# Kernel tuning notes

Measured on AMD Instinct MI355X. Metric: run time of the kernel, lower is better.

Reference implementation:

```python
import jax, jax.numpy as jnp
import numpy as np

N = 500000
E = 3000000
F = 128


def _lin_params(key, fan_in, fan_out):
    kw, kb = jax.random.split(key)
    s = 1.0 / np.sqrt(fan_in)
    w = jax.random.uniform(kw, (fan_in, fan_out), jnp.float32, -s, s)
    b = jax.random.uniform(kb, (fan_out,), jnp.float32, -s, s)
    return w, b


def setup_inputs() -> dict:
    key = jax.random.key(0)
    ks = jax.random.split(key, 16)
    hv = jax.random.normal(ks[0], (N, 7), jnp.float32)
    edge_index = jax.random.randint(ks[1], (2, E), 0, N, jnp.int32)
    mf_w0, mf_b0 = _lin_params(ks[2], 7, F)
    mf_w1, mf_b1 = _lin_params(ks[3], F, F)
    g1_rel_w, g1_rel_b = _lin_params(ks[4], F, F)
    g1_root_w, _ = _lin_params(ks[5], F, F)
    g2_rel_w, g2_rel_b = _lin_params(ks[6], F, F)
    g2_root_w, _ = _lin_params(ks[7], F, F)
    s1_w0, s1_b0 = _lin_params(ks[8], F, F)
    s1_w1, s1_b1 = _lin_params(ks[9], F, F)
    s1_w2, s1_b2 = _lin_params(ks[10], F, F)
    s2_w0, s2_b0 = _lin_params(ks[11], 2 * F, F)
    s2_w1, s2_b1 = _lin_params(ks[12], F, F)
    s2_w2, s2_b2 = _lin_params(ks[13], F, 2)
    return dict(hv=hv, edge_index=edge_index,
                mf_w0=mf_w0, mf_b0=mf_b0, mf_w1=mf_w1, mf_b1=mf_b1,
                g1_rel_w=g1_rel_w, g1_rel_b=g1_rel_b, g1_root_w=g1_root_w,
                g2_rel_w=g2_rel_w, g2_rel_b=g2_rel_b, g2_root_w=g2_root_w,
                s1_w0=s1_w0, s1_b0=s1_b0, s1_w1=s1_w1, s1_b1=s1_b1,
                s1_w2=s1_w2, s1_b2=s1_b2,
                s2_w0=s2_w0, s2_b0=s2_b0, s2_w1=s2_w1, s2_b1=s2_b1,
                s2_w2=s2_w2, s2_b2=s2_b2)


def _graph_conv(x, edge_index, rel_w, rel_b, root_w):
    # PyG GraphConv (aggr='add'): out = lin_rel(sum_{j->i} x_j) + lin_root(x_i)
    src, dst = edge_index[0], edge_index[1]
    agg = jax.ops.segment_sum(x[src], dst, num_segments=x.shape[0])
    return agg @ rel_w + rel_b + x @ root_w


def reference(hv, edge_index,
              mf_w0, mf_b0, mf_w1, mf_b1,
              g1_rel_w, g1_rel_b, g1_root_w,
              g2_rel_w, g2_rel_b, g2_root_w,
              s1_w0, s1_b0, s1_w1, s1_b1, s1_w2, s1_b2,
              s2_w0, s2_b0, s2_w1, s2_b1, s2_w2, s2_b2):
    elu = jax.nn.elu
    # mlp_face
    face_features = elu(elu(hv @ mf_w0 + mf_b0) @ mf_w1 + mf_b1)
    # gnn1
    h = _graph_conv(face_features, edge_index, g1_rel_w, g1_rel_b, g1_root_w)
    # stage1: ELU, Lin, ELU, Lin, ELU, Lin, ELU
    h = elu(elu(elu(elu(h) @ s1_w0 + s1_b0) @ s1_w1 + s1_b1) @ s1_w2 + s1_b2)
    # gnn2
    h = _graph_conv(h, edge_index, g2_rel_w, g2_rel_b, g2_root_w)
    # concat + stage2
    ef = jnp.concatenate([face_features, h], axis=-1)  # [N, 2F]
    out = elu(ef @ s2_w0 + s2_b0)
    out = elu(out @ s2_w1 + s2_b1)
    out = out @ s2_w2 + s2_b2  # [N, 2]
    # torch transpose(-1, 1) on a 2D tensor swaps dim 1 with dim 1: identity
    return out
```

## Files before the change

kernel.cpp:

```cpp
#include <hip/hip_runtime.h>
#include <hip/hip_bf16.h>
#include <hip/hip_fp16.h>
#include <type_traits>
#include <utility>


#define NROWS 500000
#define NEDGE 3000000
#define NCHUNK ((NROWS + 63) / 64)
#define NBKT 489
#define BSTR 16

typedef unsigned short u16;
using short8 = __attribute__((ext_vector_type(8))) short;
using half8  = __attribute__((ext_vector_type(8))) _Float16;
using f32x4  = __attribute__((ext_vector_type(4))) float;

__device__ __forceinline__ u16 f2h_bits(float f) {
  _Float16 h = (_Float16)f;
  return __builtin_bit_cast(u16, h);
}
__device__ __forceinline__ float h2f(u16 b) {
  return (float)__builtin_bit_cast(_Float16, b);
}
__device__ __forceinline__ float eluf(float x) { return x > 0.0f ? x : expm1f(x); }

template <typename T, typename = void> struct HasUnsafeAdd : std::false_type {};
template <typename T>
struct HasUnsafeAdd<T, std::void_t<decltype(unsafeAtomicAdd(
    std::declval<T*>(), std::declval<T>()))>> : std::true_type {};
template <bool HAS> struct AtomAdd;
template <> struct AtomAdd<true> {
  template <class T> __device__ static void go(T* p, T v) { unsafeAtomicAdd(p, v); }
};
template <> struct AtomAdd<false> {
  template <class T> __device__ static void go(T* p, T v) {
    unsigned* up = reinterpret_cast<unsigned*>(p);
    unsigned old = *up;
    while (true) {
      unsigned assumed = old;
      T cur = __builtin_bit_cast(T, assumed);
      T nw = __hadd2(cur, v);
      old = atomicCAS(up, assumed, __builtin_bit_cast(unsigned, nw));
      if (old == assumed) break;
    }
  }
};
__device__ __forceinline__ void atomAddH2(__half2* p, __half2 v) {
  AtomAdd<HasUnsafeAdd<__half2>::value>::go(p, v);
}

__global__ __launch_bounds__(256) void transpose_w(
    const float* p0, const float* p1, const float* p2, const float* p3,
    const float* p4, const float* p5, const float* p6, const float* p7,
    const float* p8, const float* p10, u16* dst)
{
  const float* src = p0; int eoff = 0;
  switch (blockIdx.y) {
    case 1: src = p1; break;  case 2: src = p2; break;
    case 3: src = p3; break;  case 4: src = p4; break;
    case 5: src = p5; break;  case 6: src = p6; break;
    case 7: src = p7; break;  case 8: src = p8; break;
    case 9: src = p8; eoff = 16384; break;
    case 10: src = p10; break;
    default: break;
  }
  u16* out = dst + (size_t)blockIdx.y * 16384;
  for (int i = threadIdx.x + blockIdx.x * 256; i < 16384; i += 2048) {
    int n = i >> 7, k = i & 127;
    out[i] = f2h_bits(src[eoff + k * 128 + n]);
  }
}

__global__ __launch_bounds__(256) void bucket_hist(const int* __restrict__ ei,
                                                   int* __restrict__ gbaseP) {
  __shared__ int cnt[512];
  int tid = threadIdx.x;
  for (int i = tid; i < 512; i += 256) cnt[i] = 0;
  __syncthreads();
  long e0 = (long)blockIdx.x * 8192;
  int n = (int)min((long)8192, (long)NEDGE - e0);
  for (int i = tid; i < n; i += 256) atomicAdd(&cnt[ei[NEDGE + e0 + i] >> 10], 1);
  __syncthreads();
  for (int b = tid; b < NBKT; b += 256)
    if (cnt[b]) atomicAdd(&gbaseP[b * BSTR], cnt[b]);
}

__global__ __launch_bounds__(512) void bucket_scan(int* gbaseP, int* gcurP) {
  __shared__ int sd[512];
  int tid = threadIdx.x;
  int v = (tid < NBKT) ? gbaseP[tid * BSTR] : 0;
  sd[tid] = v;
  __syncthreads();
  for (int off = 1; off < 512; off <<= 1) {
    int val = (tid >= off) ? sd[tid - off] : 0;
    __syncthreads();
    sd[tid] += val;
    __syncthreads();
  }
  int excl = sd[tid] - v;
  if (tid < NBKT) { gbaseP[tid * BSTR] = excl; gcurP[tid * BSTR] = excl; }
  if (tid == 0) gbaseP[NBKT * BSTR] = NEDGE;
}

__global__ __launch_bounds__(256) void partition_kernel(
    const int* __restrict__ ei, int* __restrict__ gcurP, int* __restrict__ adj)
{
  __shared__ int cnt[512], cnt2[512], rsv[512];
  int tid = threadIdx.x;
  for (int i = tid; i < 512; i += 256) { cnt[i] = 0; cnt2[i] = 0; }
  __syncthreads();
  long e0 = (long)blockIdx.x * 8192;
  int n = (int)min((long)8192, (long)NEDGE - e0);
  for (int i = tid; i < n; i += 256) atomicAdd(&cnt[ei[NEDGE + e0 + i] >> 10], 1);
  __syncthreads();
  for (int b = tid; b < NBKT; b += 256) {
    int c = cnt[b];
    rsv[b] = c ? atomicAdd(&gcurP[b * BSTR], c) : 0;
  }
  __syncthreads();
  for (int i = tid; i < n; i += 256) {
    int d = ei[NEDGE + e0 + i], s = ei[e0 + i];
    int b = d >> 10;
    int r = atomicAdd(&cnt2[b], 1);
    adj[rsv[b] + r] = ((d & 1023) << 19) | s;
  }
}

__global__ __launch_bounds__(256) void bucket_sort(
    const int* __restrict__ gbaseP, int* adj, int* __restrict__ cur,
    int* __restrict__ scratch)
{
  __shared__ __align__(16) int pk[8192];
  __shared__ __align__(16) int outb[8192];
  __shared__ int cnts[1024];
  __shared__ int base[1024];
  __shared__ int sd[256];
  int tid = threadIdx.x, b = blockIdx.x;
  int beg = gbaseP[b * BSTR], end = gbaseP[(b + 1) * BSTR];
  int cnt = end - beg;
  int n0 = b << 10;
  int nn = min(1024, NROWS - n0);
  bool fits = (cnt <= 8192);

  if (fits) {
    for (int i = tid; i < cnt; i += 256) pk[i] = adj[beg + i];
  } else {
    for (int i = tid; i < cnt; i += 256) scratch[beg + i] = adj[beg + i];
  }
  for (int i = tid; i < 1024; i += 256) cnts[i] = 0;
  __syncthreads();

  if (fits) {
    for (int i = tid; i < cnt; i += 256) atomicAdd(&cnts[pk[i] >> 19], 1);
  } else {
    for (int i = tid; i < cnt; i += 256) atomicAdd(&cnts[scratch[beg + i] >> 19], 1);
  }
  __syncthreads();

  int l0 = cnts[tid * 4], l1 = cnts[tid * 4 + 1],
      l2 = cnts[tid * 4 + 2], l3 = cnts[tid * 4 + 3];
  int p = l0 + l1 + l2 + l3;
  sd[tid] = p;
  __syncthreads();
  for (int off = 1; off < 256; off <<= 1) {
    int val = (tid >= off) ? sd[tid - off] : 0;
    __syncthreads();
    sd[tid] += val;
    __syncthreads();
  }
  int excl = sd[tid] - p;
  int lv[4] = {l0, l1, l2, l3};
#pragma unroll
  for (int k = 0; k < 4; ++k) {
    int node = tid * 4 + k;
    base[node] = excl;
    excl += lv[k];
    if (node < nn) cur[n0 + node] = beg + excl;
  }
  __syncthreads();
  for (int i = tid; i < 1024; i += 256) cnts[i] = 0;
  __syncthreads();

  if (fits) {
    for (int i = tid; i < cnt; i += 256) {
      int v = pk[i];
      int ld = v >> 19;
      int r = atomicAdd(&cnts[ld], 1);
      outb[base[ld] + r] = v & 0x7FFFF;
    }
    __syncthreads();
    for (int i = tid; i < cnt; i += 256) adj[beg + i] = outb[i];
  } else {
    for (int i = tid; i < cnt; i += 256) {
      int v = scratch[beg + i];
      int ld = v >> 19;
      int r = atomicAdd(&cnts[ld], 1);
      adj[beg + base[ld] + r] = v & 0x7FFFF;
    }
  }
}

__global__ __launch_bounds__(256) void gather_agg(
    const u16* __restrict__ x, const int* __restrict__ cend,
    const int* __restrict__ adj, u16* __restrict__ agg)
{
  int wv = threadIdx.x >> 6, lane = threadIdx.x & 63;
  long node = (long)blockIdx.x * 4 + wv;
  if (node >= NROWS) return;
  int beg = (node == 0) ? 0 : cend[node - 1];
  int end = cend[node];
  float a0 = 0.f, a1 = 0.f;
  for (int j = beg; j < end; j += 8) {
    int take = end - j;
    if (take > 8) take = 8;
    int srcv = (lane < take) ? adj[j + lane] : 0;
    unsigned hb[8];
#pragma unroll
    for (int t = 0; t < 8; ++t) {
      if (t < take) {
        int src = __shfl(srcv, t);
        hb[t] = *reinterpret_cast<const unsigned*>(x + (long)src * 128 + lane * 2);
      }
    }
#pragma unroll
    for (int t = 0; t < 8; ++t) {
      if (t < take) {
        __half2 h = __builtin_bit_cast(__half2, hb[t]);
        a0 += (float)h.x;
        a1 += (float)h.y;
      }
    }
  }
  __half2 r;
  r.x = __float2half(a0);
  r.y = __float2half(a1);
  *reinterpret_cast<__half2*>(agg + node * 128 + lane * 2) = r;
}

__global__ __launch_bounds__(256) void scatter_kernel(
    const u16* __restrict__ x, const int* __restrict__ ei,
    __half2* __restrict__ agg)
{
  int gtid = blockIdx.x * 256 + threadIdx.x;
  int wid = gtid >> 6, lane = gtid & 63;
  int nw = gridDim.x * 4;
  for (int e = wid; e < NEDGE; e += nw) {
    int s = ei[e];
    int d = ei[NEDGE + e];
    __half2 h = *reinterpret_cast<const __half2*>(x + (long)s * 128 + lane * 2);
    atomAddH2(agg + (long)d * 64 + lane, h);
  }
}

__device__ __forceinline__ void load_w_swz(const u16* Wt, short* ws, int tid) {
  for (int c = tid; c < 2048; c += 256) {
    int n = c >> 4, kb = c & 15;
    short8 v = *reinterpret_cast<const short8*>(Wt + n * 128 + kb * 8);
    *reinterpret_cast<short8*>(ws + ((n << 4) | (kb ^ (n & 15))) * 8) = v;
  }
}
__device__ __forceinline__ half8 read_b_swz(const short* ws, int col, int kb) {
  short8 v = *reinterpret_cast<const short8*>(ws + ((col << 4) | (kb ^ (col & 15))) * 8);
  return __builtin_bit_cast(half8, v);
}
__device__ __forceinline__ void gemm_global(f32x4* acc, const u16* X, long arow,
                                            bool active, const short* wbuf,
                                            int nl, int q) {
#pragma unroll
  for (int s = 0; s < 4; ++s) {
    int kofs = s * 32 + q * 8, kb = (s << 2) | q;
    half8 a = half8{0,0,0,0,0,0,0,0};
    if (active)
      a = __builtin_bit_cast(half8,
          *reinterpret_cast<const short8*>(X + arow * 128 + kofs));
#pragma unroll
    for (int c = 0; c < 8; ++c) {
      half8 b = read_b_swz(wbuf, (c << 4) | nl, kb);
      acc[c] = __builtin_amdgcn_mfma_f32_16x16x32_f16(a, b, acc[c], 0, 0, 0);
    }
  }
}
__device__ __forceinline__ void gemm_tile(f32x4* acc, const short* mytile,
                                          const short* wbuf, int nl, int q) {
#pragma unroll
  for (int s = 0; s < 4; ++s) {
    int kofs = s * 32 + q * 8, kb = (s << 2) | q;
    half8 a = __builtin_bit_cast(half8,
        *reinterpret_cast<const short8*>(&mytile[nl * 136 + kofs]));
#pragma unroll
    for (int c = 0; c < 8; ++c) {
      half8 b = read_b_swz(wbuf, (c << 4) | nl, kb);
      acc[c] = __builtin_amdgcn_mfma_f32_16x16x32_f16(a, b, acc[c], 0, 0, 0);
    }
  }
}
__device__ __forceinline__ void zero_acc(f32x4* acc) {
#pragma unroll
  for (int c = 0; c < 8; ++c) acc[c] = f32x4{0.f, 0.f, 0.f, 0.f};
}

template<bool DUAL, bool ACT>
__global__ __launch_bounds__(256) void layer_kernel(
    const u16* X, const u16* X2,
    const u16* __restrict__ W1t, const u16* __restrict__ W2t,
    const float* __restrict__ bias, u16* Y)
{
  __shared__ __align__(16) short w1s[16384];
  __shared__ __align__(16) short w2s[DUAL ? 16384 : 8];
  __shared__ float bs[128];
  int tid = threadIdx.x;
  load_w_swz(W1t, w1s, tid);
  if constexpr (DUAL) load_w_swz(W2t, w2s, tid);
  if (tid < 128) bs[tid] = bias[tid];
  __syncthreads();

  int wv = tid >> 6, lane = tid & 63, nl = lane & 15, q = lane >> 4;
  for (int ch = blockIdx.x; ch < NCHUNK; ch += gridDim.x) {
    long r0 = (long)ch * 64 + wv * 16;
    if (r0 >= NROWS) continue;
    long arow = r0 + nl;
    f32x4 acc[8];
    zero_acc(acc);
    gemm_global(acc, X, arow, true, w1s, nl, q);
    if constexpr (DUAL) gemm_global(acc, X2, arow, true, w2s, nl, q);
#pragma unroll
    for (int c = 0; c < 8; ++c) {
      float bv = bs[(c << 4) | nl];
#pragma unroll
      for (int r = 0; r < 4; ++r) {
        float o = acc[c][r] + bv;
        if constexpr (ACT) o = eluf(o);
        Y[(r0 + q * 4 + r) * 128 + ((c << 4) | nl)] = f2h_bits(o);
      }
    }
  }
}

__global__ __launch_bounds__(256) void mlp_face_kernel(
    const float* __restrict__ hv, const float* __restrict__ w0,
    const float* __restrict__ b0, const u16* __restrict__ w1t,
    const float* __restrict__ b1, u16* ff)
{
  __shared__ __align__(16) short w1s[16384];
  __shared__ __align__(16) short act0[64 * 136];
  __shared__ float hvs[448];
  __shared__ float w0s[896];
  __shared__ float b0s[128];
  __shared__ float b1s[128];
  int tid = threadIdx.x;
  load_w_swz(w1t, w1s, tid);
  for (int i = tid; i < 896; i += 256) w0s[i] = w0[i];
  if (tid < 128) { b0s[tid] = b0[tid]; b1s[tid] = b1[tid]; }
  int wv = tid >> 6, lane = tid & 63, nl = lane & 15, q = lane >> 4;

  for (int ch = blockIdx.x; ch < NCHUNK; ch += gridDim.x) {
    long base = (long)ch * 64;
    __syncthreads();
    for (int i = tid; i < 448; i += 256) {
      long g = base * 7 + i;
      hvs[i] = (g < (long)NROWS * 7) ? hv[g] : 0.0f;
    }
    __syncthreads();
    for (int idx = tid; idx < 8192; idx += 256) {
      int n = idx >> 7, c = idx & 127;
      float s = b0s[c];
#pragma unroll
      for (int k = 0; k < 7; ++k) s += hvs[n * 7 + k] * w0s[k * 128 + c];
      act0[n * 136 + c] = (short)f2h_bits(eluf(s));
    }
    __syncthreads();
    long r0 = base + wv * 16;
    if (r0 >= NROWS) continue;
    f32x4 acc[8];
    zero_acc(acc);
    gemm_tile(acc, &act0[(wv * 16) * 136], w1s, nl, q);
#pragma unroll
    for (int c = 0; c < 8; ++c) {
      float bv = b1s[(c << 4) | nl];
#pragma unroll
      for (int r = 0; r < 4; ++r)
        ff[(r0 + q * 4 + r) * 128 + ((c << 4) | nl)] = f2h_bits(eluf(acc[c][r] + bv));
    }
  }
}

__global__ __launch_bounds__(256) void final_kernel(
    const u16* __restrict__ x, const float* __restrict__ w2,
    const float* __restrict__ b2, float* __restrict__ out)
{
  __shared__ float w2s[256];
  __shared__ float b2s[2];
  int tid = threadIdx.x;
  w2s[tid] = w2[tid];
  if (tid < 2) b2s[tid] = b2[tid];
  __syncthreads();
  for (int ch = blockIdx.x; ch < NCHUNK; ch += gridDim.x) {
    long node = (long)ch * 64 + (tid >> 2);
    int q = tid & 3;
    if (node >= NROWS) continue;
    const u16* xr = x + node * 128 + q * 32;
    float p0 = 0.f, p1 = 0.f;
#pragma unroll
    for (int i = 0; i < 4; ++i) {
      short8 v = *reinterpret_cast<const short8*>(xr + i * 8);
#pragma unroll
      for (int j = 0; j < 8; ++j) {
        float f = h2f((u16)v[j]);
        int cidx = q * 32 + i * 8 + j;
        p0 += f * w2s[cidx * 2];
        p1 += f * w2s[cidx * 2 + 1];
      }
    }
    p0 += __shfl_xor(p0, 1); p0 += __shfl_xor(p0, 2);
    p1 += __shfl_xor(p1, 1); p1 += __shfl_xor(p1, 2);
    if (q == 0) {
      out[node * 2]     = p0 + b2s[0];
      out[node * 2 + 1] = p1 + b2s[1];
    }
  }
}

extern "C" void kernel_launch(void* const* d_in, const int* in_sizes, int n_in,
                              void* d_out, int out_size, void* d_ws, size_t ws_size,
                              hipStream_t stream) {
  const float* hv        = (const float*)d_in[0];
  const int*   ei        = (const int*)d_in[1];
  const float* mf_w0     = (const float*)d_in[2];
  const float* mf_b0     = (const float*)d_in[3];
  const float* mf_w1     = (const float*)d_in[4];
  const float* mf_b1     = (const float*)d_in[5];
  const float* g1_rel_w  = (const float*)d_in[6];
  const float* g1_rel_b  = (const float*)d_in[7];
  const float* g1_root_w = (const float*)d_in[8];
  const float* g2_rel_w  = (const float*)d_in[9];
  const float* g2_rel_b  = (const float*)d_in[10];
  const float* g2_root_w = (const float*)d_in[11];
  const float* s1_w0     = (const float*)d_in[12];
  const float* s1_b0     = (const float*)d_in[13];
  const float* s1_w1     = (const float*)d_in[14];
  const float* s1_b1     = (const float*)d_in[15];
  const float* s1_w2     = (const float*)d_in[16];
  const float* s1_b2     = (const float*)d_in[17];
  const float* s2_w0     = (const float*)d_in[18];
  const float* s2_b0     = (const float*)d_in[19];
  const float* s2_w1     = (const float*)d_in[20];
  const float* s2_b1     = (const float*)d_in[21];
  const float* s2_w2     = (const float*)d_in[22];
  const float* s2_b2     = (const float*)d_in[23];

  constexpr size_t ACT_BYTES = (size_t)NROWS * 128 * 2;
  constexpr size_t ADJ_BYTES = (size_t)NEDGE * 4;
  constexpr size_t WT_BYTES  = 11 * 16384 * 2;
  constexpr size_t CSR_NEED  = 2 * ACT_BYTES + ADJ_BYTES + WT_BYTES + 4096;

  char* ws = (char*)d_ws;
  u16* A   = (u16*)ws;
  u16* G   = (u16*)(ws + ACT_BYTES);
  int* adj = (int*)(ws + 2 * ACT_BYTES);
  const bool CSRP = ws_size >= CSR_NEED;

  u16* wT;
  int* cur;
  int* gbaseP;
  int* gcurP;
  if (CSRP) {
    wT     = (u16*)(ws + 2 * ACT_BYTES + ADJ_BYTES);
    cur    = (int*)d_out;
    gbaseP = (int*)((char*)d_out + 2000000);
    gcurP  = (int*)((char*)d_out + 2000000 + (NBKT + 1) * 64);
  } else {
    wT     = (u16*)d_out;
    cur    = nullptr; gbaseP = nullptr; gcurP = nullptr;
  }

  u16* mf_w1T   = wT + 0 * 16384;
  u16* g1_relT  = wT + 1 * 16384;
  u16* g1_rootT = wT + 2 * 16384;
  u16* s1_w0T   = wT + 3 * 16384;
  u16* s1_w1T   = wT + 4 * 16384;
  u16* s1_w2T   = wT + 5 * 16384;
  u16* g2_relT  = wT + 6 * 16384;
  u16* g2_rootT = wT + 7 * 16384;
  u16* s2w0loT  = wT + 8 * 16384;
  u16* s2w0hiT  = wT + 9 * 16384;
  u16* s2_w1T   = wT + 10 * 16384;

  transpose_w<<<dim3(8, 11), 256, 0, stream>>>(
      mf_w1, g1_rel_w, g1_root_w, s1_w0, s1_w1, s1_w2,
      g2_rel_w, g2_root_w, s2_w0, s2_w1, wT);

  const int gS = 1024;
  const int gD = 512;
  const int gM = 512;
  const int gF = 1024;
  const int gT = (NEDGE + 8191) / 8192;
  const int gn = (NROWS + 3) / 4;

  if (CSRP) {
    (void)hipMemsetAsync(gbaseP, 0, (size_t)(2 * NBKT + 1) * 64, stream);
    bucket_hist<<<gT, 256, 0, stream>>>(ei, gbaseP);
    bucket_scan<<<1, 512, 0, stream>>>(gbaseP, gcurP);
    partition_kernel<<<gT, 256, 0, stream>>>(ei, gcurP, adj);
    bucket_sort<<<NBKT, 256, 0, stream>>>(gbaseP, adj, cur, (int*)G);

    mlp_face_kernel<<<gM, 256, 0, stream>>>(hv, mf_w0, mf_b0, mf_w1T, mf_b1, A);
    gather_agg<<<gn, 256, 0, stream>>>(A, cur, adj, G);
    layer_kernel<true,  true ><<<gD, 256, 0, stream>>>(G, A, g1_relT, g1_rootT, g1_rel_b, A);
    layer_kernel<false, true ><<<gS, 256, 0, stream>>>(A, nullptr, s1_w0T, nullptr, s1_b0, A);
    layer_kernel<false, true ><<<gS, 256, 0, stream>>>(A, nullptr, s1_w1T, nullptr, s1_b1, A);
    layer_kernel<false, true ><<<gS, 256, 0, stream>>>(A, nullptr, s1_w2T, nullptr, s1_b2, A);
    gather_agg<<<gn, 256, 0, stream>>>(A, cur, adj, G);
    layer_kernel<true,  false><<<gD, 256, 0, stream>>>(G, A, g2_relT, g2_rootT, g2_rel_b, A);
    mlp_face_kernel<<<gM, 256, 0, stream>>>(hv, mf_w0, mf_b0, mf_w1T, mf_b1, G);
    layer_kernel<true,  true ><<<gD, 256, 0, stream>>>(G, A, s2w0loT, s2w0hiT, s2_b0, G);
    layer_kernel<false, true ><<<gS, 256, 0, stream>>>(G, nullptr, s2_w1T, nullptr, s2_b1, G);
    final_kernel<<<gF, 256, 0, stream>>>(G, s2_w2, s2_b2, (float*)d_out);
  } else {
    mlp_face_kernel<<<gM, 256, 0, stream>>>(hv, mf_w0, mf_b0, mf_w1T, mf_b1, A);
    (void)hipMemsetAsync(G, 0, ACT_BYTES, stream);
    scatter_kernel<<<4096, 256, 0, stream>>>(A, ei, (__half2*)G);
    layer_kernel<true,  true ><<<gD, 256, 0, stream>>>(G, A, g1_relT, g1_rootT, g1_rel_b, A);
    layer_kernel<false, true ><<<gS, 256, 0, stream>>>(A, nullptr, s1_w0T, nullptr, s1_b0, A);
    layer_kernel<false, true ><<<gS, 256, 0, stream>>>(A, nullptr, s1_w1T, nullptr, s1_b1, A);
    layer_kernel<false, true ><<<gS, 256, 0, stream>>>(A, nullptr, s1_w2T, nullptr, s1_b2, A);
    (void)hipMemsetAsync(G, 0, ACT_BYTES, stream);
    scatter_kernel<<<4096, 256, 0, stream>>>(A, ei, (__half2*)G);
    layer_kernel<true,  false><<<gD, 256, 0, stream>>>(G, A, g2_relT, g2_rootT, g2_rel_b, A);
    mlp_face_kernel<<<gM, 256, 0, stream>>>(hv, mf_w0, mf_b0, mf_w1T, mf_b1, G);
    layer_kernel<true,  true ><<<gD, 256, 0, stream>>>(G, A, s2w0loT, s2w0hiT, s2_b0, G);
    layer_kernel<false, true ><<<gS, 256, 0, stream>>>(G, nullptr, s2_w1T, nullptr, s2_b1, G);
    final_kernel<<<gF, 256, 0, stream>>>(G, s2_w2, s2_b2, (float*)d_out);
  }
}
```

Baseline: 1.445 ms.

## Process four nodes per wave in gather and fuse last layer with final projection

```diff
diff --git a/kernel.cpp b/kernel.cpp
--- a/kernel.cpp
+++ b/kernel.cpp
@@ -206,36 +206,56 @@
     const int* __restrict__ adj, u16* __restrict__ agg)
 {
   int wv = threadIdx.x >> 6, lane = threadIdx.x & 63;
-  long node = (long)blockIdx.x * 4 + wv;
-  if (node >= NROWS) return;
-  int beg = (node == 0) ? 0 : cend[node - 1];
-  int end = cend[node];
-  float a0 = 0.f, a1 = 0.f;
-  for (int j = beg; j < end; j += 8) {
-    int take = end - j;
-    if (take > 8) take = 8;
-    int srcv = (lane < take) ? adj[j + lane] : 0;
-    unsigned hb[8];
-#pragma unroll
-    for (int t = 0; t < 8; ++t) {
-      if (t < take) {
-        int src = __shfl(srcv, t);
-        hb[t] = *reinterpret_cast<const unsigned*>(x + (long)src * 128 + lane * 2);
-      }
-    }
-#pragma unroll
-    for (int t = 0; t < 8; ++t) {
-      if (t < take) {
-        __half2 h = __builtin_bit_cast(__half2, hb[t]);
-        a0 += (float)h.x;
-        a1 += (float)h.y;
-      }
-    }
-  }
-  __half2 r;
-  r.x = __float2half(a0);
-  r.y = __float2half(a1);
-  *reinterpret_cast<__half2*>(agg + node * 128 + lane * 2) = r;
+  long n0 = ((long)blockIdx.x * 4 + wv) * 4;
+  if (n0 >= NROWS) return;
+  int cval = 0;
+  if (lane < 5) {
+    long idx = n0 - 1 + lane;
+    cval = (idx >= 0) ? cend[idx] : 0;
+  }
+  int b[5];
+#pragma unroll
+  for (int k = 0; k < 5; ++k) b[k] = __shfl(cval, k);
+  int deg[4];
+#pragma unroll
+  for (int n = 0; n < 4; ++n) deg[n] = b[n + 1] - b[n];
+  int maxdeg = max(max(deg[0], deg[1]), max(deg[2], deg[3]));
+
+  float a0[4] = {0.f, 0.f, 0.f, 0.f}, a1[4] = {0.f, 0.f, 0.f, 0.f};
+  for (int off = 0; off < maxdeg; off += 8) {
+    int sv[4], dn[4];
+#pragma unroll
+    for (int n = 0; n < 4; ++n) {
+      dn[n] = min(max(deg[n] - off, 0), 8);
+      sv[n] = (lane < dn[n]) ? adj[b[n] + off + lane] : 0;
+    }
+    unsigned hb[4][8];
+#pragma unroll
+    for (int n = 0; n < 4; ++n)
+#pragma unroll
+      for (int t = 0; t < 8; ++t)
+        if (t < dn[n]) {
+          int src = __shfl(sv[n], t);
+          hb[n][t] = *reinterpret_cast<const unsigned*>(
+              x + (long)src * 128 + lane * 2);
+        }
+#pragma unroll
+    for (int n = 0; n < 4; ++n)
+#pragma unroll
+      for (int t = 0; t < 8; ++t)
+        if (t < dn[n]) {
+          __half2 h = __builtin_bit_cast(__half2, hb[n][t]);
+          a0[n] += (float)h.x;
+          a1[n] += (float)h.y;
+        }
+  }
+#pragma unroll
+  for (int n = 0; n < 4; ++n) {
+    __half2 r;
+    r.x = __float2half(a0[n]);
+    r.y = __float2half(a1[n]);
+    *reinterpret_cast<__half2*>(agg + (n0 + n) * 128 + lane * 2) = r;
+  }
 }
 
 __global__ __launch_bounds__(256) void scatter_kernel(
@@ -332,6 +352,60 @@
         float o = acc[c][r] + bv;
         if constexpr (ACT) o = eluf(o);
         Y[(r0 + q * 4 + r) * 128 + ((c << 4) | nl)] = f2h_bits(o);
+      }
+    }
+  }
+}
+
+__global__ __launch_bounds__(256) void layer_final_kernel(
+    const u16* __restrict__ X, const u16* __restrict__ W1t,
+    const float* __restrict__ bias, const float* __restrict__ w2,
+    const float* __restrict__ b2, float* __restrict__ out)
+{
+  __shared__ __align__(16) short w1s[16384];
+  __shared__ float bs[128];
+  __shared__ float w2s[256];
+  __shared__ float b2s[2];
+  int tid = threadIdx.x;
+  load_w_swz(W1t, w1s, tid);
+  if (tid < 128) bs[tid] = bias[tid];
+  w2s[tid] = w2[tid];
+  if (tid < 2) b2s[tid] = b2[tid];
+  __syncthreads();
+
+  int wv = tid >> 6, lane = tid & 63, nl = lane & 15, q = lane >> 4;
+  for (int ch = blockIdx.x; ch < NCHUNK; ch += gridDim.x) {
+    long r0 = (long)ch * 64 + wv * 16;
+    if (r0 >= NROWS) continue;
+    long arow = r0 + nl;
+    f32x4 acc[8];
+    zero_acc(acc);
+    gemm_global(acc, X, arow, true, w1s, nl, q);
+    float pr[4][2] = {{0.f,0.f},{0.f,0.f},{0.f,0.f},{0.f,0.f}};
+#pragma unroll
+    for (int c = 0; c < 8; ++c) {
+      int col = (c << 4) | nl;
+      float bv = bs[col];
+      float w20 = w2s[col * 2], w21 = w2s[col * 2 + 1];
+#pragma unroll
+      for (int r = 0; r < 4; ++r) {
+        float o = eluf(acc[c][r] + bv);
+        pr[r][0] += o * w20;
+        pr[r][1] += o * w21;
+      }
+    }
+#pragma unroll
+    for (int r = 0; r < 4; ++r)
+#pragma unroll
+      for (int m = 1; m < 16; m <<= 1) {
+        pr[r][0] += __shfl_xor(pr[r][0], m);
+        pr[r][1] += __shfl_xor(pr[r][1], m);
+      }
+    if (nl == 0) {
+#pragma unroll
+      for (int r = 0; r < 4; ++r) {
+        out[(r0 + q * 4 + r) * 2]     = pr[r][0] + b2s[0];
+        out[(r0 + q * 4 + r) * 2 + 1] = pr[r][1] + b2s[1];
       }
     }
   }
@@ -495,7 +569,7 @@
   const int gM = 512;
   const int gF = 1024;
   const int gT = (NEDGE + 8191) / 8192;
-  const int gn = (NROWS + 3) / 4;
+  const int gn = (NROWS + 15) / 16;
 
   if (CSRP) {
     (void)hipMemsetAsync(gbaseP, 0, (size_t)(2 * NBKT + 1) * 64, stream);
@@ -514,8 +588,8 @@
     layer_kernel<true,  false><<<gD, 256, 0, stream>>>(G, A, g2_relT, g2_rootT, g2_rel_b, A);
     mlp_face_kernel<<<gM, 256, 0, stream>>>(hv, mf_w0, mf_b0, mf_w1T, mf_b1, G);
     layer_kernel<true,  true ><<<gD, 256, 0, stream>>>(G, A, s2w0loT, s2w0hiT, s2_b0, G);
-    layer_kernel<false, true ><<<gS, 256, 0, stream>>>(G, nullptr, s2_w1T, nullptr, s2_b1, G);
-    final_kernel<<<gF, 256, 0, stream>>>(G, s2_w2, s2_b2, (float*)d_out);
+    layer_final_kernel<<<gS, 256, 0, stream>>>(G, s2_w1T, s2_b1, s2_w2, s2_b2,
+                                               (float*)d_out);
   } else {
     mlp_face_kernel<<<gM, 256, 0, stream>>>(hv, mf_w0, mf_b0, mf_w1T, mf_b1, A);
     (void)hipMemsetAsync(G, 0, ACT_BYTES, stream);
```

Result: slower. 1.701 ms (+17.7%).
